# Performance work log

Hardware: AMD Instinct MI355X
Metric: run time of the kernel (lower is better)

Reference implementation:

```python
import jax, jax.numpy as jnp
from jax import lax
import numpy as np

UNITS = 256
DYN = 32
STATIC = 27


def setup_inputs() -> dict:
    key = jax.random.key(0)
    ks = jax.random.split(key, 7)
    x_dynamic = jax.random.normal(ks[0], (1024, 365, DYN), dtype=jnp.float32)
    x_static = jax.random.normal(ks[1], (1024, STATIC), dtype=jnp.float32)
    # learned parameters (orthogonal-ish init approximated by scaled normals;
    # weight_hh initialized as tiled identity per the original module)
    weight_ih = jax.random.normal(ks[2], (DYN, 3 * UNITS), dtype=jnp.float32) * 0.1
    eye3 = jnp.concatenate([jnp.eye(UNITS, dtype=jnp.float32)] * 3, axis=1)
    weight_hh = eye3 + jax.random.normal(ks[3], (UNITS, 3 * UNITS), dtype=jnp.float32) * 0.02
    weight_sh = jax.random.normal(ks[4], (STATIC, UNITS), dtype=jnp.float32) * 0.1
    bias = jnp.zeros((3 * UNITS,), dtype=jnp.float32)
    bias_s = jnp.zeros((UNITS,), dtype=jnp.float32)
    return {
        "x_dynamic": x_dynamic,
        "x_static": x_static,
        "weight_ih": weight_ih,
        "weight_hh": weight_hh,
        "weight_sh": weight_sh,
        "bias": bias,
        "bias_s": bias_s,
    }


def reference(x_dynamic, x_static, weight_ih, weight_hh, weight_sh, bias, bias_s):
    B = x_dynamic.shape[0]
    U = weight_sh.shape[1]
    # static input gate, computed once (entity-aware)
    i_gate = jax.nn.sigmoid(x_static @ weight_sh + bias_s)  # [B, U]
    # precompute input contribution for all timesteps: [B, T, 3U]
    gx = jnp.einsum("btd,dk->btk", x_dynamic, weight_ih) + bias
    gx_t = jnp.swapaxes(gx, 0, 1)  # [T, B, 3U] for scan

    h0 = jnp.zeros((B, U), dtype=x_dynamic.dtype)
    c0 = jnp.zeros((B, U), dtype=x_dynamic.dtype)

    def step(carry, g_t):
        h, c = carry
        gates = g_t + h @ weight_hh  # [B, 3U]
        f, o, g = jnp.split(gates, 3, axis=1)
        c_new = jax.nn.sigmoid(f) * c + i_gate * jnp.tanh(g)
        h_new = jax.nn.sigmoid(o) * jnp.tanh(c_new)
        return (h_new, c_new), None

    (h_final, c_final), _ = lax.scan(step, (h0, c0), gx_t)
    return h_final
```

## Files before the change

kernel.cpp:

```cpp
#include <hip/hip_runtime.h>


typedef short short8 __attribute__((ext_vector_type(8)));
typedef short short4s __attribute__((ext_vector_type(4)));
typedef float f32x4 __attribute__((ext_vector_type(4)));
typedef int   i32x4 __attribute__((ext_vector_type(4)));

#define T_STEPS 365
#define UNITS   256
#define G3      768
#define MROWS   4
#define NWGS    256
#define HP8     288
#define XROW    (T_STEPS * 32)
#define WP8_BYTES (256 * G3)

__device__ __forceinline__ unsigned short f2bf(float x) {
    union { float f; unsigned u; } v; v.f = x;
    return (unsigned short)((v.u + 0x7FFFu + ((v.u >> 16) & 1u)) >> 16);
}
__device__ __forceinline__ float rcp_(float x) {
    float r; asm("v_rcp_f32 %0, %1" : "=v"(r) : "v"(x)); return r;
}
__device__ __forceinline__ float sigm_(float x) {
    return rcp_(1.0f + __expf(-x));
}
__device__ __forceinline__ float tanh_(float x) {
    return 1.0f - 2.0f * rcp_(1.0f + __expf(2.0f * x));
}
__device__ __forceinline__ f32x4 MF(short8 a, short8 b, f32x4 c) {
    return __builtin_amdgcn_mfma_f32_16x16x32_bf16(a, b, c, 0, 0, 0);
}
__device__ __forceinline__ i32x4 MI(i32x4 a, i32x4 b, i32x4 c) {
    return __builtin_amdgcn_mfma_i32_16x16x64_i8(a, b, c, 0, 0, 0);
}

__global__ __launch_bounds__(256) void pack_weights(
    const float* __restrict__ w_ih, const float* __restrict__ w_hh,
    signed char* __restrict__ wp8, unsigned short* __restrict__ wpx)
{
    int idx = blockIdx.x * 256 + threadIdx.x;
    if (idx < 256 * G3) {
        const int k = idx / G3, n = idx - k * G3;
        float v = w_hh[k * G3 + n];
        if ((n & 255) == k) v -= 1.0f;
        int q = (int)rintf(v * 1024.0f);
        q = q > 127 ? 127 : (q < -127 ? -127 : q);
        wp8[((size_t)((k >> 6) * G3) + n) * 64 + (k & 63)] = (signed char)q;
    } else if (idx < (256 + 32) * G3) {
        const int idx2 = idx - 256 * G3;
        const int kx = idx2 / G3, n = idx2 - kx * G3;
        wpx[((size_t)((kx >> 3) * G3) + n) * 8 + (kx & 7)] = f2bf(w_ih[kx * G3 + n]);
    }
}

#define STEP_BODY(T, FC, FN, DONEXT) do {                                     \
    const int p_ = (T) & 1;                                                   \
    __syncthreads();                                                          \
    const signed char* Ap_ = &A_s[p_][0][0];                                  \
    const i32x4 a0_ = *(const i32x4*)(Ap_ + abase);                           \
    const i32x4 a1_ = *(const i32x4*)(Ap_ + abase + 64);                      \
    const i32x4 a2_ = *(const i32x4*)(Ap_ + abase + 128);                     \
    const i32x4 a3_ = *(const i32x4*)(Ap_ + abase + 192);                     \
        \
    i32x4 if0_ = MI(a0_, bwi[0][0][0], IZERO);                                \
    i32x4 io0_ = MI(a0_, bwi[0][1][0], IZERO);                                \
    i32x4 ig0_ = MI(a0_, bwi[0][2][0], IZERO);                                \
    if0_ = MI(a1_, bwi[1][0][0], if0_);                                       \
    io0_ = MI(a1_, bwi[1][1][0], io0_);                                       \
    ig0_ = MI(a1_, bwi[1][2][0], ig0_);                                       \
    if0_ = MI(a2_, bwi[2][0][0], if0_);                                       \
    io0_ = MI(a2_, bwi[2][1][0], io0_);                                       \
    ig0_ = MI(a2_, bwi[2][2][0], ig0_);                                       \
    if0_ = MI(a3_, bwi[3][0][0], if0_);                                       \
    io0_ = MI(a3_, bwi[3][1][0], io0_);                                       \
    ig0_ = MI(a3_, bwi[3][2][0], ig0_);                                       \
    i32x4 if1_ = MI(a0_, bwi[0][0][1], IZERO);                                \
    i32x4 io1_ = MI(a0_, bwi[0][1][1], IZERO);                                \
    i32x4 ig1_ = MI(a0_, bwi[0][2][1], IZERO);                                \
    if1_ = MI(a1_, bwi[1][0][1], if1_);                                       \
    io1_ = MI(a1_, bwi[1][1][1], io1_);                                       \
    ig1_ = MI(a1_, bwi[1][2][1], ig1_);                                       \
    if1_ = MI(a2_, bwi[2][0][1], if1_);                                       \
    io1_ = MI(a2_, bwi[2][1][1], io1_);                                       \
    ig1_ = MI(a2_, bwi[2][2][1], ig1_);                                       \
    if1_ = MI(a3_, bwi[3][0][1], if1_);                                       \
    io1_ = MI(a3_, bwi[3][1][1], io1_);                                       \
    ig1_ = MI(a3_, bwi[3][2][1], ig1_);                                       \
    if (DONEXT) {                                                             \
            \
        const short8 xu_ = xa;                                                \
        FN[0] = MF(xu_, bwx[0][0], FZERO);                                    \
        FN[1] = MF(xu_, bwx[1][0], FZERO);                                    \
        FN[2] = MF(xu_, bwx[2][0], FZERO);                                    \
        FN[3] = MF(xu_, bwx[0][1], FZERO);                                    \
        FN[4] = MF(xu_, bwx[1][1], FZERO);                                    \
        FN[5] = MF(xu_, bwx[2][1], FZERO);                                    \
        const int tn_ = ((T) + 2 < T_STEPS) ? (T) + 2 : T_STEPS - 1;          \
        xa = *(const short8*)(xp + (size_t)tn_ * 32);                         \
    }                                                                         \
    {                       \
        const float bh_ = hp[0];                                              \
        const float gf_ = FC[0][0] + bfv[0] + bh_ + (float)if0_[0] * SCL;     \
        const float go_ = FC[1][0] + bov[0] + bh_ + (float)io0_[0] * SCL;     \
        const float gg_ = FC[2][0] + bgv[0] + bh_ + (float)ig0_[0] * SCL;     \
        const float f_  = sigm_(gf_);                                         \
        const float o_  = sigm_(go_);                                         \
        const float gt_ = tanh_(gg_);                                         \
        const float cn_ = f_ * cc[0] + ig[0] * gt_;                           \
        cc[0] = cn_;                                                          \
        const float hn_ = o_ * tanh_(cn_);                                    \
        hp[0] = hn_;                                                          \
        A_s[p_ ^ 1][qq][u0] = (signed char)__float2int_rn(hn_ * 127.0f);      \
    }                                                                         \
    {                                                           \
        const float bh_ = hp[1];                                              \
        const float gf_ = FC[3][0] + bfv[1] + bh_ + (float)if1_[0] * SCL;     \
        const float go_ = FC[4][0] + bov[1] + bh_ + (float)io1_[0] * SCL;     \
        const float gg_ = FC[5][0] + bgv[1] + bh_ + (float)ig1_[0] * SCL;     \
        const float f_  = sigm_(gf_);                                         \
        const float o_  = sigm_(go_);                                         \
        const float gt_ = tanh_(gg_);                                         \
        const float cn_ = f_ * cc[1] + ig[1] * gt_;                           \
        cc[1] = cn_;                                                          \
        const float hn_ = o_ * tanh_(cn_);                                    \
        hp[1] = hn_;                                                          \
        A_s[p_ ^ 1][qq][u1] = (signed char)__float2int_rn(hn_ * 127.0f);      \
    }                                                                         \
} while (0)

__global__ __launch_bounds__(512, 2) void lstm_mfma(
    const float* __restrict__ x_dyn,
    const float* __restrict__ x_sta,
    const signed char* __restrict__ wp8,
    const unsigned short* __restrict__ wpx,
    const float* __restrict__ w_sh,
    const float* __restrict__ bias,
    const float* __restrict__ bias_s,
    float* __restrict__ out)
{
    __shared__ signed char A_s[2][MROWS][HP8];
    __shared__ unsigned short xs[MROWS * XROW];

    const int tid  = threadIdx.x;
    const int b0   = blockIdx.x * MROWS;
    const int lane = tid & 63;
    const int wv   = tid >> 6;
    const int mm   = lane & 15;
    const int qq   = lane >> 4;

    i32x4 bwi[4][3][2];
    #pragma unroll
    for (int ks = 0; ks < 4; ++ks)
        #pragma unroll
        for (int g = 0; g < 3; ++g)
            #pragma unroll
            for (int h = 0; h < 2; ++h) {
                const int n = g * UNITS + wv * 32 + h * 16 + mm;
                bwi[ks][g][h] = *(const i32x4*)(wp8 +
                    ((size_t)(ks * G3) + n) * 64 + qq * 16);
            }
    short8 bwx[3][2];
    #pragma unroll
    for (int g = 0; g < 3; ++g)
        #pragma unroll
        for (int h = 0; h < 2; ++h)
            bwx[g][h] = *(const short8*)(wpx +
                ((size_t)(qq * G3) + g * UNITS + wv * 32 + h * 16 + mm) * 8);

    #pragma unroll
    for (int r = 0; r < MROWS; ++r) {
        const float4* src = (const float4*)(x_dyn + (size_t)(b0 + r) * XROW);
        short4s* dst = (short4s*)(xs + r * XROW);
        for (int i = tid; i < XROW / 4; i += 512) {
            const float4 v = src[i];
            short4s w;
            w.x = (short)f2bf(v.x); w.y = (short)f2bf(v.y);
            w.z = (short)f2bf(v.z); w.w = (short)f2bf(v.w);
            dst[i] = w;
        }
    }
    {
        int* az = (int*)A_s;
        for (int i = tid; i < 2 * MROWS * HP8 / 4; i += 512) az[i] = 0;
    }
    __syncthreads();

    const int u0 = wv * 32 + mm;
    const int u1 = u0 + 16;

    const float bfv[2] = { bias[u0],             bias[u1] };
    const float bov[2] = { bias[UNITS + u0],     bias[UNITS + u1] };
    const float bgv[2] = { bias[2 * UNITS + u0], bias[2 * UNITS + u1] };

    float ig[2], cc[2], hp[2];
    #pragma unroll
    for (int h = 0; h < 2; ++h) {
        const int u = h ? u1 : u0;
        float s = bias_s[u];
        #pragma unroll
        for (int j = 0; j < 27; ++j)
            s += x_sta[(b0 + qq) * 27 + j] * w_sh[j * UNITS + u];
        ig[h] = sigm_(s);
        cc[h] = 0.0f; hp[h] = 0.0f;
    }

    const int arow  = (mm >> 2);
    const int abase = arow * HP8 + qq * 16;
    const unsigned short* xp = xs + (size_t)arow * XROW + qq * 8;
    const float SCL = 1.0f / (127.0f * 1024.0f);
    const f32x4 FZERO = {0.f, 0.f, 0.f, 0.f};
    const i32x4 IZERO = {0, 0, 0, 0};

    f32x4 FA[6], FB[6];
    short8 xa;
    {
        const short8 x0 = *(const short8*)(xp);
        FA[0] = MF(x0, bwx[0][0], FZERO);
        FA[1] = MF(x0, bwx[1][0], FZERO);
        FA[2] = MF(x0, bwx[2][0], FZERO);
        FA[3] = MF(x0, bwx[0][1], FZERO);
        FA[4] = MF(x0, bwx[1][1], FZERO);
        FA[5] = MF(x0, bwx[2][1], FZERO);
        xa = *(const short8*)(xp + 32);
    }

    for (int i = 0; i < 182; ++i) {
        STEP_BODY(2 * i,     FA, FB, true);
        STEP_BODY(2 * i + 1, FB, FA, true);
    }
    STEP_BODY(364, FA, FB, false);

    out[(size_t)(b0 + qq) * UNITS + u0] = hp[0];
    out[(size_t)(b0 + qq) * UNITS + u1] = hp[1];
}

extern "C" void kernel_launch(void* const* d_in, const int* in_sizes, int n_in,
                              void* d_out, int out_size, void* d_ws, size_t ws_size,
                              hipStream_t stream) {
    const float* x_dyn  = (const float*)d_in[0];
    const float* x_sta  = (const float*)d_in[1];
    const float* w_ih   = (const float*)d_in[2];
    const float* w_hh   = (const float*)d_in[3];
    const float* w_sh   = (const float*)d_in[4];
    const float* bias   = (const float*)d_in[5];
    const float* bias_s = (const float*)d_in[6];
    float* out = (float*)d_out;
    signed char* wp8 = (signed char*)d_ws;
    unsigned short* wpx = (unsigned short*)((char*)d_ws + WP8_BYTES);

    pack_weights<<<((256 + 32) * G3 + 255) / 256, 256, 0, stream>>>(w_ih, w_hh, wp8, wpx);
    lstm_mfma<<<NWGS, 512, 0, stream>>>(x_dyn, x_sta, wp8, wpx, w_sh, bias, bias_s, out);
}
```

Before: 369.7 us.

## Batch input projection MFMA over four timesteps per window

Instead of issuing six input-projection MFMAs every timestep with only element 0 used, the x tile is laid out so one MFMA computes four consecutive timesteps, using accumulator element E for step E of a 4-step window. This cuts input-projection MFMA work and LDS loads by four, and the x buffer gets zero padding so the final window can read past the end. In exchange the step body now carries per-window state and the loop is unrolled more heavily, which may raise register pressure.

```diff
diff --git a/kernel.cpp b/kernel.cpp
--- a/kernel.cpp
+++ b/kernel.cpp
@@ -13,6 +13,7 @@
 #define NWGS    256
 #define HP8     288
 #define XROW    (T_STEPS * 32)
+#define XPAD    96
 #define WP8_BYTES (256 * G3)
 
 __device__ __forceinline__ unsigned short f2bf(float x) {
@@ -54,8 +55,8 @@
     }
 }
 
-#define STEP_BODY(T, FC, FN, DONEXT) do {                                     \
-    const int p_ = (T) & 1;                                                   \
+#define STEP_BODY(E, FC, FN, DOX, LOADX, W) do {                              \
+    const int p_ = (E) & 1;                                                   \
     __syncthreads();                                                          \
     const signed char* Ap_ = &A_s[p_][0][0];                                  \
     const i32x4 a0_ = *(const i32x4*)(Ap_ + abase);                           \
@@ -87,8 +88,8 @@
     if1_ = MI(a3_, bwi[3][0][1], if1_);                                       \
     io1_ = MI(a3_, bwi[3][1][1], io1_);                                       \
     ig1_ = MI(a3_, bwi[3][2][1], ig1_);                                       \
-    if (DONEXT) {                                                             \
-            \
+    if (DOX) {                                                                \
+           \
         const short8 xu_ = xa;                                                \
         FN[0] = MF(xu_, bwx[0][0], FZERO);                                    \
         FN[1] = MF(xu_, bwx[1][0], FZERO);                                    \
@@ -96,14 +97,14 @@
         FN[3] = MF(xu_, bwx[0][1], FZERO);                                    \
         FN[4] = MF(xu_, bwx[1][1], FZERO);                                    \
         FN[5] = MF(xu_, bwx[2][1], FZERO);                                    \
-        const int tn_ = ((T) + 2 < T_STEPS) ? (T) + 2 : T_STEPS - 1;          \
-        xa = *(const short8*)(xp + (size_t)tn_ * 32);                         \
+        if (LOADX)                                                            \
+            xa = *(const short8*)(xq + (size_t)((W) + 2) * 128);              \
     }                                                                         \
-    {                       \
+    {         \
         const float bh_ = hp[0];                                              \
-        const float gf_ = FC[0][0] + bfv[0] + bh_ + (float)if0_[0] * SCL;     \
-        const float go_ = FC[1][0] + bov[0] + bh_ + (float)io0_[0] * SCL;     \
-        const float gg_ = FC[2][0] + bgv[0] + bh_ + (float)ig0_[0] * SCL;     \
+        const float gf_ = FC[0][E] + bfv[0] + bh_ + (float)if0_[0] * SCL;     \
+        const float go_ = FC[1][E] + bov[0] + bh_ + (float)io0_[0] * SCL;     \
+        const float gg_ = FC[2][E] + bgv[0] + bh_ + (float)ig0_[0] * SCL;     \
         const float f_  = sigm_(gf_);                                         \
         const float o_  = sigm_(go_);                                         \
         const float gt_ = tanh_(gg_);                                         \
@@ -115,9 +116,9 @@
     }                                                                         \
     {                                                           \
         const float bh_ = hp[1];                                              \
-        const float gf_ = FC[3][0] + bfv[1] + bh_ + (float)if1_[0] * SCL;     \
-        const float go_ = FC[4][0] + bov[1] + bh_ + (float)io1_[0] * SCL;     \
-        const float gg_ = FC[5][0] + bgv[1] + bh_ + (float)ig1_[0] * SCL;     \
+        const float gf_ = FC[3][E] + bfv[1] + bh_ + (float)if1_[0] * SCL;     \
+        const float go_ = FC[4][E] + bov[1] + bh_ + (float)io1_[0] * SCL;     \
+        const float gg_ = FC[5][E] + bgv[1] + bh_ + (float)ig1_[0] * SCL;     \
         const float f_  = sigm_(gf_);                                         \
         const float o_  = sigm_(go_);                                         \
         const float gt_ = tanh_(gg_);                                         \
@@ -127,6 +128,13 @@
         hp[1] = hn_;                                                          \
         A_s[p_ ^ 1][qq][u1] = (signed char)__float2int_rn(hn_ * 127.0f);      \
     }                                                                         \
+} while (0)
+
+#define WINDOW4(W, FC, FN, LOADX) do {                                        \
+    STEP_BODY(0, FC, FN, false, false, W);                                    \
+    STEP_BODY(1, FC, FN, true,  LOADX, W);                                    \
+    STEP_BODY(2, FC, FN, false, false, W);                                    \
+    STEP_BODY(3, FC, FN, false, false, W);                                    \
 } while (0)
 
 __global__ __launch_bounds__(512, 2) void lstm_mfma(
@@ -140,7 +148,7 @@
     float* __restrict__ out)
 {
     __shared__ signed char A_s[2][MROWS][HP8];
-    __shared__ unsigned short xs[MROWS * XROW];
+    __shared__ unsigned short xs[MROWS * XROW + XPAD];
 
     const int tid  = threadIdx.x;
     const int b0   = blockIdx.x * MROWS;
@@ -180,6 +188,7 @@
             dst[i] = w;
         }
     }
+    if (tid < XPAD / 2) ((int*)(xs + MROWS * XROW))[tid] = 0;
     {
         int* az = (int*)A_s;
         for (int i = tid; i < 2 * MROWS * HP8 / 4; i += 512) az[i] = 0;
@@ -205,9 +214,8 @@
         cc[h] = 0.0f; hp[h] = 0.0f;
     }
 
-    const int arow  = (mm >> 2);
-    const int abase = arow * HP8 + qq * 16;
-    const unsigned short* xp = xs + (size_t)arow * XROW + qq * 8;
+    const int abase = (mm >> 2) * HP8 + qq * 16;
+    const unsigned short* xq = xs + (size_t)(mm >> 2) * XROW + (mm & 3) * 32 + qq * 8;
     const float SCL = 1.0f / (127.0f * 1024.0f);
     const f32x4 FZERO = {0.f, 0.f, 0.f, 0.f};
     const i32x4 IZERO = {0, 0, 0, 0};
@@ -215,21 +223,23 @@
     f32x4 FA[6], FB[6];
     short8 xa;
     {
-        const short8 x0 = *(const short8*)(xp);
+        const short8 x0 = *(const short8*)(xq);
         FA[0] = MF(x0, bwx[0][0], FZERO);
         FA[1] = MF(x0, bwx[1][0], FZERO);
         FA[2] = MF(x0, bwx[2][0], FZERO);
         FA[3] = MF(x0, bwx[0][1], FZERO);
         FA[4] = MF(x0, bwx[1][1], FZERO);
         FA[5] = MF(x0, bwx[2][1], FZERO);
-        xa = *(const short8*)(xp + 32);
-    }
-
-    for (int i = 0; i < 182; ++i) {
-        STEP_BODY(2 * i,     FA, FB, true);
-        STEP_BODY(2 * i + 1, FB, FA, true);
-    }
-    STEP_BODY(364, FA, FB, false);
+        xa = *(const short8*)(xq + 128);
+    }
+
+    for (int wp = 0; wp < 45; ++wp) {
+        const int w0 = wp * 2;
+        WINDOW4(w0,     FA, FB, true);
+        WINDOW4(w0 + 1, FB, FA, true);
+    }
+    WINDOW4(90, FA, FB, false);
+    STEP_BODY(0, FB, FA, false, false, 91);
 
     out[(size_t)(b0 + qq) * UNITS + u0] = hp[0];
     out[(size_t)(b0 + qq) * UNITS + u1] = hp[1];
```

Result: faster. 348.9 us (median of 2 runs) (-5.6%).
